# Kernel optimization log

Hardware: AMD Instinct MI355X
Metric: run time of the kernel (lower is better)

The kernel has to match this reference:

```python
import jax, jax.numpy as jnp
import numpy as np


def conv1d(x, w, b):
    # x: (N, Cin, W), w: (Cout, Cin, K) -> (N, Cout, W-K+1), VALID conv (torch Conv1d)
    y = jax.lax.conv_general_dilated(x, w, (1,), 'VALID', dimension_numbers=('NCH', 'OIH', 'NCH'))
    return y + b[None, :, None]


def cnn_block(x, w, b):
    # conv1d then MaxPool1d over the full valid length -> (N, Cout)
    return jnp.max(conv1d(x, w, b), axis=2)


def highway(x, Wp, bp, Wg, bg):
    p = jax.nn.relu(x @ Wp.T + bp)
    g = jax.nn.sigmoid(x @ Wg.T + bg)
    return g * p + (1.0 - g) * x


def lstm_masked(x, lens, Wih, Whh, bih, bhh):
    # x: (N, Wt, E); lens: (N,) valid lengths. Emulates pack_padded_sequence +
    # nn.LSTM + pad_packed_sequence: outputs are h_t for t < len, zeros after.
    N, Wt, _ = x.shape
    H = Whh.shape[1]
    bias = bih + bhh
    h0 = jnp.zeros((N, H), x.dtype)

    def step(carry, inp):
        xt, t = inp
        h, c = carry
        z = xt @ Wih.T + h @ Whh.T + bias  # (N, 4H), gate order i,f,g,o
        i, f, g, o = jnp.split(z, 4, axis=-1)
        c2 = jax.nn.sigmoid(f) * c + jax.nn.sigmoid(i) * jnp.tanh(g)
        h2 = jax.nn.sigmoid(o) * jnp.tanh(c2)
        valid = (t < lens)[:, None]
        h2 = jnp.where(valid, h2, h)
        c2 = jnp.where(valid, c2, c)
        return (h2, c2), jnp.where(valid, h2, jnp.zeros_like(h2))

    xs = jnp.moveaxis(x, 1, 0)  # (Wt, N, E)
    ts = jnp.arange(Wt)
    _, out = jax.lax.scan(step, (h0, h0), (xs, ts))
    return jnp.moveaxis(out, 0, 1)  # (N, Wt, H)


def setup_inputs() -> dict:
    key = jax.random.key(0)
    ks = jax.random.split(key, 32)
    B, T = 32, 48
    WL, WA, WE = 33, 50, 30
    EL, EA, EE, H = 300, 988, 20, 128
    CL, CA, CE = 128, 256, 64
    s = 0.02
    inp = {
        'x_lin': jax.random.normal(ks[0], (B, T, WL, EL), jnp.float32),
        'x_aco': jax.random.normal(ks[1], (B, T, WA, EA), jnp.float32),
        'x_emo': jax.random.normal(ks[2], (B, T, WE, EE), jnp.float32),
        'window_length': jax.random.randint(ks[3], (B, T), 0, WE).astype(jnp.int32) + 1,
        'length': jax.random.randint(ks[4], (B,), 1, T + 1).astype(jnp.int32),
        # CNN params
        'convL_w': s * jax.random.normal(ks[5], (CL, EL, 5), jnp.float32),
        'convL_b': jnp.zeros((CL,), jnp.float32),
        'convA_w': s * jax.random.normal(ks[6], (CA, EA, 10), jnp.float32),
        'convA_b': jnp.zeros((CA,), jnp.float32),
        'convE_w': s * jax.random.normal(ks[7], (CE, H, 3), jnp.float32),
        'convE_b': jnp.zeros((CE,), jnp.float32),
        # Highway params
        'hwL_Wp': s * jax.random.normal(ks[8], (CL, CL), jnp.float32),
        'hwL_bp': jnp.zeros((CL,), jnp.float32),
        'hwL_Wg': s * jax.random.normal(ks[9], (CL, CL), jnp.float32),
        'hwL_bg': jnp.zeros((CL,), jnp.float32),
        'hwA_Wp': s * jax.random.normal(ks[10], (CA, CA), jnp.float32),
        'hwA_bp': jnp.zeros((CA,), jnp.float32),
        'hwA_Wg': s * jax.random.normal(ks[11], (CA, CA), jnp.float32),
        'hwA_bg': jnp.zeros((CA,), jnp.float32),
        'hwE_Wp': s * jax.random.normal(ks[12], (CE, CE), jnp.float32),
        'hwE_bp': jnp.zeros((CE,), jnp.float32),
        'hwE_Wg': s * jax.random.normal(ks[13], (CE, CE), jnp.float32),
        'hwE_bg': jnp.zeros((CE,), jnp.float32),
        # LSTM params (nn.LSTM, 1 layer, batch_first)
        'lstm_Wih': s * jax.random.normal(ks[14], (4 * H, EE), jnp.float32),
        'lstm_Whh': s * jax.random.normal(ks[15], (4 * H, H), jnp.float32),
        'lstm_bih': jnp.zeros((4 * H,), jnp.float32),
        'lstm_bhh': jnp.zeros((4 * H,), jnp.float32),
    }
    return inp


def reference(x_lin, x_aco, x_emo, window_length, length,
              convL_w, convL_b, convA_w, convA_b, convE_w, convE_b,
              hwL_Wp, hwL_bp, hwL_Wg, hwL_bg,
              hwA_Wp, hwA_bp, hwA_Wg, hwA_bg,
              hwE_Wp, hwE_bp, hwE_Wg, hwE_bg,
              lstm_Wih, lstm_Whh, lstm_bih, lstm_bhh):
    B, T = x_lin.shape[:2]
    # Linguistic: per-window CNN + Highway (dropout = identity in eval)
    xl = x_lin.reshape(B * T, x_lin.shape[2], x_lin.shape[3]).transpose(0, 2, 1)  # (BT, 300, WL)
    outL = highway(cnn_block(xl, convL_w, convL_b), hwL_Wp, hwL_bp, hwL_Wg, hwL_bg)
    outL = outL.reshape(B, T, -1)
    # Acoustic
    xa = x_aco.reshape(B * T, x_aco.shape[2], x_aco.shape[3]).transpose(0, 2, 1)  # (BT, 988, WA)
    outA = highway(cnn_block(xa, convA_w, convA_b), hwA_Wp, hwA_bp, hwA_Wg, hwA_bg)
    outA = outA.reshape(B, T, -1)
    # Emotient: ragged per-window LSTM (packed semantics) -> CNN -> Highway
    xe = x_emo.reshape(B * T, x_emo.shape[2], x_emo.shape[3])  # (BT, WE, 20)
    lens = window_length.reshape(B * T)
    h = lstm_masked(xe, lens, lstm_Wih, lstm_Whh, lstm_bih, lstm_bhh)  # (BT, WE, 128)
    outE = highway(cnn_block(h.transpose(0, 2, 1), convE_w, convE_b), hwE_Wp, hwE_bp, hwE_Wg, hwE_bg)
    outE = outE.reshape(B, T, -1)
    # Concatenate modalities -> (B, T, 128+256+64) fed to the downstream head
    return jnp.concatenate([outL, outA, outE], axis=2)
```

## Files before the change

kernel.cpp:

```cpp
#include <hip/hip_runtime.h>
#include <hip/hip_bf16.h>
#include <math.h>

#define BTOT 1536
#define EL 300
#define ELP 320
#define WL_ 33
#define CL 128
#define LOUTL 29
#define KPL 1600
#define EA 988
#define EAP 992
#define WA_ 50
#define CA 256
#define LOUTA 41
#define KPA 9920
#define EE 20
#define WE_ 30
#define HH 128
#define CE 64
#define LOUTE 28
#define KPE 384
#define KDIML 1500
#define KDIMA 9880
// ... 5 lines not shown
__device__ __forceinline__ unsigned short f2bf(float f) {
    unsigned int x = __float_as_uint(f);
    unsigned int r = (x + 0x7fffu + ((x >> 16) & 1u)) >> 16;
    return (unsigned short)r;
}

__device__ __forceinline__ float sigmf(float x) {
    return __builtin_amdgcn_rcpf(1.f + __expf(-x));
}
__device__ __forceinline__ float tanh_fast(float x) {
    return 1.f - 2.f * __builtin_amdgcn_rcpf(1.f + __expf(2.f * x));
}

#define GLD16(gp, lp) __builtin_amdgcn_global_load_lds( \
    (const __attribute__((address_space(1))) void*)(gp), \
    (__attribute__((address_space(3))) void*)(lp), 16, 0, 0)

template<int N> __device__ __forceinline__ void vmwait() {
    if constexpr (N == 0) asm volatile("s_waitcnt vmcnt(0)" ::: "memory");
    else if constexpr (N == 1) asm volatile("s_waitcnt vmcnt(1)" ::: "memory");
    else if constexpr (N == 2) asm volatile("s_waitcnt vmcnt(2)" ::: "memory");
    else if constexpr (N == 3) asm volatile("s_waitcnt vmcnt(3)" ::: "memory");
    else if constexpr (N == 4) asm volatile("s_waitcnt vmcnt(4)" ::: "memory");
    else if constexpr (N == 5) asm volatile("s_waitcnt vmcnt(5)" ::: "memory");
    else if constexpr (N == 6) asm volatile("s_waitcnt vmcnt(6)" ::: "memory");
    else if constexpr (N == 8) asm volatile("s_waitcnt vmcnt(8)" ::: "memory");
    else static_assert(N == 0, "add case");
}

__device__ __forceinline__ void tr_one(const float* a, float* at, int R, int C, int idx) {
    int r = idx / C, c = idx - r * C;
    at[c * R + r] = a[idx];
}
template<int CIN, int CINP, int KW, int COUT, int KPAD>
__device__ __forceinline__ void wt_one(const float* w, unsigned short* wt, int idx) {
    int co = idx / KPAD;
    int p  = idx - co * KPAD;
    int k  = p / CINP;
    int c  = p - k * CINP;
    float v = 0.f;
    if (k < KW && c < CIN) v = w[(co * CIN + c) * KW + k];
    wt[idx] = f2bf(v);
}
template<bool BIG>
__global__ void prep_all(const float* hwL_Wp, float* WpTL, const float* hwL_Wg, float* WgTL,
                         const float* hwA_Wp, float* WpTA, const float* hwA_Wg, float* WgTA,
                         const float* hwE_Wp, float* WpTE, const float* hwE_Wg, float* WgTE,
                         const float* lstm_Wih, float* WihT, const float* lstm_Whh, float* WhhT,
                         const float* convL_w, unsigned short* wtL,
                         const float* convE_w, unsigned short* wtE,
                         const float* convA_w, unsigned short* wtA,
                         unsigned short* whh_bf, unsigned short* wihp_bf) {
    constexpr int S1 = 16384, S2 = 16384, S3 = 65536, S4 = 65536, S5 = 4096, S6 = 4096;
    constexpr int S7 = 512 * 20, S8 = 512 * 128;
    constexpr int S9 = 128 * KPL, S10 = 64 * KPE, S11 = 512 * 128, S12 = 512 * 32;
    constexpr int S13 = CA * KPA;
    constexpr int SMALL = S1 + S2 + S3 + S4 + S5 + S6 + S7 + S8;
    constexpr int TOTAL = BIG ? (SMALL + S9 + S10 + S11 + S12 + S13) : SMALL;
    int stride = gridDim.x * blockDim.x;
    for (int i = blockIdx.x * blockDim.x + threadIdx.x; i < TOTAL; i += stride) {
        int idx = i;
        if (idx < S1) { tr_one(hwL_Wp, WpTL, 128, 128, idx); continue; } idx -= S1;
        if (idx < S2) { tr_one(hwL_Wg, WgTL, 128, 128, idx); continue; } idx -= S2;
        if (idx < S3) { tr_one(hwA_Wp, WpTA, 256, 256, idx); continue; } idx -= S3;
        if (idx < S4) { tr_one(hwA_Wg, WgTA, 256, 256, idx); continue; } idx -= S4;
        if (idx < S5) { tr_one(hwE_Wp, WpTE, 64, 64, idx); continue; } idx -= S5;
        if (idx < S6) { tr_one(hwE_Wg, WgTE, 64, 64, idx); continue; } idx -= S6;
        if (idx < S7) { tr_one(lstm_Wih, WihT, 512, 20, idx); continue; } idx -= S7;
        if (idx < S8) { tr_one(lstm_Whh, WhhT, 512, 128, idx); continue; } idx -= S8;
        if constexpr (BIG) {
            if (idx < S9) { wt_one<EL, ELP, 5, CL, KPL>(convL_w, wtL, idx); continue; } idx -= S9;
            if (idx < S10) { wt_one<HH, HH, 3, CE, KPE>(convE_w, wtE, idx); continue; } idx -= S10;
            if (idx < S11) { whh_bf[idx] = f2bf(lstm_Whh[idx]); continue; } idx -= S11;
            if (idx < S12) { int col = idx >> 5, e = idx & 31;
                             wihp_bf[idx] = (e < 20) ? f2bf(lstm_Wih[col * 20 + e]) : (unsigned short)0;
                             continue; } idx -= S12;
            wt_one<EA, EAP, 10, CA, KPA>(convA_w, wtA, idx);
        }
    }
}

template<int CIN, int CINP>
__device__ __forceinline__ void cvt_chunk(const float* in, unsigned short* out, int idx) {
    constexpr int CH = CINP / 8;
    int row = idx / CH, c0 = (idx - row * CH) * 8;
    const float* src = in + (size_t)row * CIN + c0;
    union { short8 s; unsigned short u[8]; } o;
    if (c0 + 8 <= CIN) {
        float4 v0 = *(const float4*)src;
        float4 v1 = *(const float4*)(src + 4);
        o.u[0]=f2bf(v0.x); o.u[1]=f2bf(v0.y); o.u[2]=f2bf(v0.z); o.u[3]=f2bf(v0.w);
        o.u[4]=f2bf(v1.x); o.u[5]=f2bf(v1.y); o.u[6]=f2bf(v1.z); o.u[7]=f2bf(v1.w);
    } else {
        #pragma unroll
        for (int j = 0; j < 8; ++j) o.u[j] = (c0 + j < CIN) ? f2bf(src[j]) : (unsigned short)0;
    }
    *(short8*)(out + (size_t)row * CINP + c0) = o.s;
}

#define LSTM_BLOCKS 96
#define CVTA_BLOCKS 1440

__global__ __launch_bounds__(512, 1)
void lstm_cvt(const float* __restrict__ x_emo,
              const unsigned short* __restrict__ wihp_bf, const unsigned short* __restrict__ whh_bf,
              const float* __restrict__ bih, const float* __restrict__ bhh,
              const int* __restrict__ lens, unsigned short* __restrict__ hbuf,
              const float* __restrict__ xa, unsigned short* __restrict__ outa)
{
    __shared__ __align__(16) unsigned short xq[WE_ * 16 * 32];
    __shared__ __align__(16) char h_s[2 * 16 * HH * 2];

    if (blockIdx.x >= LSTM_BLOCKS) {
        constexpr int NAC = (BTOT * WA_) * (EAP / 8);
        int stride = CVTA_BLOCKS * 512;
        for (int i = (blockIdx.x - LSTM_BLOCKS) * 512 + threadIdx.x; i < NAC; i += stride)
            cvt_chunk<EA, EAP>(xa, outa, i);
        return;
    }

    const int tid  = threadIdx.x;
    const int w    = tid >> 6;
    const int lane = tid & 63;
    const int lr   = lane & 15;
    const int lq   = lane >> 4;
    const int s0   = blockIdx.x * 16;
    const int c    = w * 16 + lr;

    short8 bfr[4][4];
    short8 bw[4];
    float bj[4];
    #pragma unroll
    for (int g = 0; g < 4; ++g) {
        int col = g * 128 + c;
        #pragma unroll
        for (int kt = 0; kt < 4; ++kt)
            bfr[g][kt] = *(const short8*)(whh_bf + (size_t)col * 128 + kt * 32 + lq * 8);
        bw[g] = *(const short8*)(wihp_bf + (size_t)col * 32 + lq * 8);
        bj[g] = bih[col] + bhh[col];
    }
    int len4[4];
    #pragma unroll
    for (int j = 0; j < 4; ++j) len4[j] = lens[s0 + lq * 4 + j];

    for (int i = tid; i < WE_ * 16 * 32; i += 512) {
        int t = i >> 9, r = (i >> 5) & 15, e = i & 31;
        xq[i] = (e < 20) ? f2bf(x_emo[(((size_t)(s0 + r) * WE_) + t) * 20 + e]) : (unsigned short)0;
    }
    for (int i = tid; i < 2048; i += 512) ((unsigned int*)h_s)[i] = 0u;

    float c_prev[4] = {0.f, 0.f, 0.f, 0.f};
    unsigned short hb_prev[4] = {0, 0, 0, 0};
    __syncthreads();

    for (int t = 0; t < WE_; ++t) {
        const char* hsr = h_s + (t & 1) * 4096;
        char* hsw = h_s + ((t & 1) ^ 1) * 4096;
        short8 ax = *(const short8*)((const char*)xq + (size_t)(t * 16 + lr) * 64 + lq * 16);
        short8 af[4];
        #pragma unroll
        for (int kt = 0; kt < 4; ++kt)
// ... 10 lines not shown
        #pragma unroll
        for (int j = 0; j < 4; ++j) {
            int s = lq * 4 + j;
            float zi = acc[0][j] + bj[0];
            float zf = acc[1][j] + bj[1];
            float zg = acc[2][j] + bj[2];
            float zo = acc[3][j] + bj[3];
            float si = sigmf(zi), sf = sigmf(zf), so = sigmf(zo);
            float tg = tanh_fast(zg);
            float c2 = sf * c_prev[j] + si * tg;
            float h2 = so * tanh_fast(c2);
            bool valid = (t < len4[j]);
            c_prev[j] = valid ? c2 : c_prev[j];
            unsigned short h2b = f2bf(h2);
            unsigned short hn = valid ? h2b : hb_prev[j];
            hb_prev[j] = hn;
            *(unsigned short*)(hsw + (((s * HH + c) * 2) ^ ((s & 7) << 4))) = hn;
            hbuf[(((size_t)(s0 + s) * WE_) + t) * HH + c] = valid ? h2b : (unsigned short)0;
        }
        __syncthreads();
    }
}

#define CONVA_BLOCKS 768
#define CVTL_BLOCKS 512
__global__ __launch_bounds__(256, 2)
void conv_a_v11(const unsigned short* __restrict__ xb, const unsigned short* __restrict__ wt,
                const float* __restrict__ bias, float* __restrict__ pooled,
                const float* __restrict__ xl, unsigned short* __restrict__ outl)
{
    constexpr int LOUT = LOUTA, WIN = WA_, CINP = EAP, BN = 128, COUT = CA;
    constexpr int CCH  = CINP / 32;
    constexpr int KB   = CINP * 2;
    constexpr int KTOTB = CINP * 10 * 2;
    constexpr int ABUF = 4 * 64 * 64;
    constexpr int BBUF = BN * 64;
    constexpr int CPQ  = 96;

    __shared__ __align__(16) char smem[2 * ABUF + 5 * BBUF];

    if (blockIdx.x >= CONVA_BLOCKS) {
        constexpr int NLC = (BTOT * WL_) * (ELP / 8);
        int stride = CVTL_BLOCKS * 256;
        for (int i = (blockIdx.x - CONVA_BLOCKS) * 256 + threadIdx.x; i < NLC; i += stride)
            cvt_chunk<EL, ELP>(xl, outl, i);
        return;
    }

    const int tid  = threadIdx.x;
    const int lane = tid & 63;
    const int wid  = tid >> 6;
    const int lr   = lane & 15;
    const int lq   = lane >> 4;
    const int lq16 = lq * 16;

    int xcd = blockIdx.x & 7;
    int n = xcd & 1;
    int m = (xcd >> 1) * CPQ + (blockIdx.x >> 3);

    f32x4 acc[3][8];
    #pragma unroll
    for (int i = 0; i < 3; ++i)
        #pragma unroll
        for (int j = 0; j < 8; ++j) acc[i][j] = (f32x4){0.f, 0.f, 0.f, 0.f};

    const int aw_r = tid >> 2;
    const int aw   = (aw_r < WIN) ? aw_r : (WIN - 1);
    const int slot = tid & 3;
    const char* asrc[4];
    #pragma unroll
    for (int i = 0; i < 4; ++i)
        asrc[i] = (const char*)xb + ((size_t)((m * 4 + i) * WIN + aw)) * KB
                + ((slot * 16) ^ (((aw_r >> 1) & 3) << 4));
    const char* bsrc[2];
    #pragma unroll
    for (int i = 0; i < 2; ++i) {
        int col = (tid + i * 256) >> 2;
        bsrc[i] = (const char*)wt + (size_t)(n * BN + col) * KTOTB
                + ((slot * 16) ^ (((col >> 1) & 3) << 4));
    }

// ... 87 lines not shown
    }
#undef VSTEP

    const int bt = m * 4 + wid;
    #pragma unroll
    for (int nf = 0; nf < 8; ++nf) {
        float mx = -INFINITY;
        #pragma unroll
        for (int o = 0; o < 3; ++o) {
            int rb = o * 16 + lq * 4;
            #pragma unroll
            for (int j = 0; j < 4; ++j)
                if (rb + j < LOUT) mx = fmaxf(mx, acc[o][nf][j]);
        }
        mx = fmaxf(mx, __shfl_xor(mx, 16, 64));
        mx = fmaxf(mx, __shfl_xor(mx, 32, 64));
        if (lane < 16) {
            int col = n * BN + nf * 16 + lane;
            pooled[(size_t)bt * COUT + col] = mx + bias[col];
        }
    }
}

template<int LOUT, int WIN, int CINP, int KW, int BN, int NS, int MFR, int COUT>
__global__ __launch_bounds__(256, 2)
void conv_pool_v10(const unsigned short* __restrict__ xb, const unsigned short* __restrict__ wt,
                   const float* __restrict__ bias, float* __restrict__ pooled)
{
    constexpr int CCH   = CINP / 32;
    constexpr int KB    = CINP * 2;
    constexpr int KTOTB = CINP * KW * 2;
    constexpr int NFR   = BN / 16;
    constexpr int B_IT  = BN / 64;
    constexpr int ABUF  = 4 * 64 * 64;
    constexpr int BBUF  = BN * 64;
    constexpr int CPQ   = (BTOT / 4) / 4;

    __shared__ __align__(16) char smem[2 * ABUF + 4 * BBUF];

    const int tid  = threadIdx.x;
    const int lane = tid & 63;
    const int wid  = tid >> 6;
    const int lr   = lane & 15;
    const int lq   = lane >> 4;
    const int lq16 = lq * 16;

    int m, n;
    if constexpr (NS == 2) {
        int xcd = blockIdx.x & 7;
        n = xcd & 1;
        m = (xcd >> 1) * CPQ + (blockIdx.x >> 3);
    } else {
        m = blockIdx.x; n = 0;
    }

    f32x4 acc[MFR][NFR];
    #pragma unroll
    for (int i = 0; i < MFR; ++i)
        #pragma unroll
        for (int j = 0; j < NFR; ++j) acc[i][j] = (f32x4){0.f, 0.f, 0.f, 0.f};

    const int aw_r = tid >> 2;
    const int aw   = (aw_r < WIN) ? aw_r : (WIN - 1);
    const int slot = tid & 3;
    const char* asrc[4];
    #pragma unroll
    for (int i = 0; i < 4; ++i)
        asrc[i] = (const char*)xb + ((size_t)((m * 4 + i) * WIN + aw)) * KB
                + ((slot * 16) ^ (((aw_r >> 1) & 3) << 4));
    const char* bsrc[B_IT];
    #pragma unroll
    for (int i = 0; i < B_IT; ++i) {
        int col = (tid + i * 256) >> 2;
        bsrc[i] = (const char*)wt + (size_t)(n * BN + col) * KTOTB
                + ((slot * 16) ^ (((col >> 1) & 3) << 4));
    }

    char* const abuf0 = smem;
    char* const abuf1 = smem + ABUF;
    char* const bbase = smem + 2 * ABUF;

    int cbo[NFR];
    #pragma unroll
    for (int nf = 0; nf < NFR; ++nf) {
        int cb = nf * 16 + lr;
        cbo[nf] = cb * 64 + (lq16 ^ (((cb >> 1) & 3) << 4));
    }

    #pragma unroll
    for (int i = 0; i < 4; ++i)
        GLD16(asrc[i], abuf0 + i * 4096 + tid * 16);
    #pragma unroll
    for (int s = 0; s < 3; ++s)
        #pragma unroll
        for (int i = 0; i < B_IT; ++i)
            GLD16(bsrc[i] + s * KB, bbase + s * BBUF + i * 4096 + tid * 16);
    vmwait<0>();
    __builtin_amdgcn_s_barrier();

    int bcur = 0;

#define STEP(KK, WN, TAIL) do {                                                    \
    const char* bb = bbase + bcur * BBUF;                                          \
    short8 afr[MFR];                                                               \
    _Pragma("unroll")                                                              \
    for (int o = 0; o < MFR; ++o) {                                                \
        int row = o * 16 + lr + (KK);                                              \
        afr[o] = *(const short8*)(awave + row * 64 + (lq16 ^ (((row >> 1) & 3) << 4))); \
    }                                                                              \
    short8 bf[NFR];                                                                \
    _Pragma("unroll")                                                              \
    for (int nf = 0; nf < NFR; ++nf) bf[nf] = *(const short8*)(bb + cbo[nf]);      \
    if (!(TAIL) || (KK) < KW - 3) {                                                \
        constexpr int k3_ = ((KK) + 3 < KW) ? (KK) + 3 : (KK) + 3 - KW;            \
        int boff = k3_ * KB + (((KK) + 3 < KW) ? ci : ci + 1) * 64;                \
        char* bstg = bbase + ((bcur + 3) & 3) * BBUF;                              \
        _Pragma("unroll")                                                          \
        for (int i = 0; i < B_IT; ++i)                                             \
            GLD16(bsrc[i] + boff, bstg + i * 4096 + tid * 16);                     \
    }                                                                              \
    if (!(TAIL)) {                                                                 \
        if (KW >= 8) {                                                             \
            if ((KK) < 4)                                                          \
                GLD16(asrc[(KK) & 3] + (size_t)(ci + 1) * 64, abn + ((KK) & 3) * 4096 + tid * 16); \
        } else if ((KK) == 0) {                                                    \
            _Pragma("unroll")                                                      \
            for (int i = 0; i < 4; ++i)                                            \
                GLD16(asrc[i] + (size_t)(ci + 1) * 64, abn + i * 4096 + tid * 16); \
        }                                                                          \
    }                                                                              \
    __builtin_amdgcn_s_setprio(1);                                                 \
    _Pragma("unroll")                                                              \
    for (int nf = 0; nf < NFR; ++nf)                                               \
        _Pragma("unroll")                                                          \
        for (int o = 0; o < MFR; ++o)                                              \
            acc[o][nf] = __builtin_amdgcn_mfma_f32_16x16x32_bf16(afr[o], bf[nf], acc[o][nf], 0, 0, 0); \
    __builtin_amdgcn_s_setprio(0);                                                 \
    vmwait<WN>();                                                                  \
    asm volatile("" ::: "memory");                                                 \
    __builtin_amdgcn_s_barrier();                                                  \
    bcur = (bcur + 1) & 3;                                                         \
} while (0)

    for (int ci = 0; ci < CCH - 1; ++ci) {
        const char* ab = (ci & 1) ? abuf1 : abuf0;
        char* abn = (ci & 1) ? abuf0 : abuf1;
        const char* awave = ab + wid * 4096;
        if constexpr (KW == 5) {
            STEP(0, 8, false); STEP(1, 8, false); STEP(2, 4, false); STEP(3, 4, false); STEP(4, 4, false);
        } else {
            STEP(0, 6, false); STEP(1, 6, false); STEP(2, 2, false);
        }
    }
    {
        const int ci = CCH - 1;
        const char* ab = (ci & 1) ? abuf1 : abuf0;
        char* abn = (ci & 1) ? abuf0 : abuf1; (void)abn;
        const char* awave = ab + wid * 4096;
        if constexpr (KW == 5) {
            STEP(0, 4, true); STEP(1, 4, true); STEP(2, 2, true); STEP(3, 0, true); STEP(4, 0, true);
        } else {
            STEP(0, 1, true); STEP(1, 0, true); STEP(2, 0, true);
        }
    }
#undef STEP

    const int bt = m * 4 + wid;
    #pragma unroll
    for (int nf = 0; nf < NFR; ++nf) {
        float mx = -INFINITY;
        #pragma unroll
        for (int o = 0; o < MFR; ++o) {
            int rb = o * 16 + lq * 4;
            #pragma unroll
            for (int j = 0; j < 4; ++j)
                if (rb + j < LOUT) mx = fmaxf(mx, acc[o][nf][j]);
        }
        mx = fmaxf(mx, __shfl_xor(mx, 16, 64));
        mx = fmaxf(mx, __shfl_xor(mx, 32, 64));
        if (lane < 16) {
            int col = n * BN + nf * 16 + lane;
            pooled[(size_t)bt * COUT + col] = mx + bias[col];
        }
    }
}

#define HWA_BLOCKS 192
#define HWL_BLOCKS 96
#define HWE_BLOCKS 48
__global__ __launch_bounds__(256)
void highway_v2(const float* __restrict__ pL, const float* __restrict__ pA, const float* __restrict__ pE,
                const float* __restrict__ WpTL, const float* __restrict__ bpL,
                const float* __restrict__ WgTL, const float* __restrict__ bgL,
                const float* __restrict__ WpTA, const float* __restrict__ bpA,
                const float* __restrict__ WgTA, const float* __restrict__ bgA,
                const float* __restrict__ WpTE, const float* __restrict__ bpE,
                const float* __restrict__ WgTE, const float* __restrict__ bgE,
                float* __restrict__ out) {
    __shared__ float xs[2048];
    int bx = blockIdx.x;
    int tid = threadIdx.x;
    if (bx < HWA_BLOCKS) {
        int bt0 = bx * 8;
        #pragma unroll
        for (int s = 0; s < 8; ++s) xs[s * 256 + tid] = pA[(size_t)(bt0 + s) * 256 + tid];
        __syncthreads();
// ... 38 lines not shown
        }
    } else {
        int bt0 = (bx - HWA_BLOCKS - HWL_BLOCKS) * 32;
        for (int i = tid; i < 32 * 64; i += 256) xs[i] = pE[(size_t)bt0 * 64 + i];
        __syncthreads();
        int j = tid & 63, grp = tid >> 6;
        float p[8], g[8];
        #pragma unroll
        for (int s = 0; s < 8; ++s) { p[s] = bpE[j]; g[s] = bgE[j]; }
        for (int c = 0; c < 64; ++c) {
            float wp = WpTE[c * 64 + j], wg = WgTE[c * 64 + j];
            #pragma unroll
            for (int s = 0; s < 8; ++s) {
                float xv = xs[(grp * 8 + s) * 64 + c];
                p[s] += xv * wp; g[s] += xv * wg;
            }
        }
        #pragma unroll
        for (int s = 0; s < 8; ++s) {
            float pp = fmaxf(p[s], 0.f);
            float gg = sigmf(g[s]);
            out[(size_t)(bt0 + grp * 8 + s) * 448 + 384 + j] = gg * pp + (1.f - gg) * xs[(grp * 8 + s) * 64 + j];
        }
    }
}

__global__ __launch_bounds__(512)
void lstm_kernel_f32(const float* __restrict__ x, const int* __restrict__ lens,
                     const float* __restrict__ WihT, const float* __restrict__ WhhT,
                     const float* __restrict__ bih, const float* __restrict__ bhh,
                     float* __restrict__ hout) {
    int bt = blockIdx.x;
    int j  = threadIdx.x;
    __shared__ float xs[WE_][EE];
    __shared__ __align__(16) float hs[HH];
    __shared__ float zs[512];
    for (int idx = j; idx < WE_ * EE; idx += 512)
        ((float*)xs)[idx] = x[(size_t)bt * WE_ * EE + idx];
    if (j < HH) hs[j] = 0.f;
    float wih[EE];
    #pragma unroll
    for (int e = 0; e < EE; ++e) wih[e] = WihT[e * 512 + j];
    float whh[HH];
    #pragma unroll
    for (int h = 0; h < HH; ++h) whh[h] = WhhT[h * 512 + j];
    float bjv = bih[j] + bhh[j];
// ... 84 lines not shown
    const float* hwA_Wg = (const float*)d_in[17];
    const float* hwA_bg = (const float*)d_in[18];
    const float* hwE_Wp = (const float*)d_in[19];
    const float* hwE_bp = (const float*)d_in[20];
    const float* hwE_Wg = (const float*)d_in[21];
    const float* hwE_bg = (const float*)d_in[22];
    const float* lstm_Wih = (const float*)d_in[23];
    const float* lstm_Whh = (const float*)d_in[24];
    const float* lstm_bih = (const float*)d_in[25];
    const float* lstm_bhh = (const float*)d_in[26];
    float* out = (float*)d_out;

    char* p0 = (char*)d_ws;
    char* p = p0;
    auto alloc = [&](size_t bytes) { char* r = p; p += (bytes + 255) & ~(size_t)255; return r; };
    float* WpTL = (float*)alloc((size_t)CL * CL * 4);
    float* WgTL = (float*)alloc((size_t)CL * CL * 4);
    float* WpTA = (float*)alloc((size_t)CA * CA * 4);
    float* WgTA = (float*)alloc((size_t)CA * CA * 4);
    float* WpTE = (float*)alloc((size_t)CE * CE * 4);
    float* WgTE = (float*)alloc((size_t)CE * CE * 4);
    float* WihT = (float*)alloc((size_t)EE * 512 * 4);
    float* WhhT = (float*)alloc((size_t)HH * 512 * 4);
    unsigned short* whh_bf  = (unsigned short*)alloc((size_t)512 * 128 * 2);
    unsigned short* wihp_bf = (unsigned short*)alloc((size_t)512 * 32 * 2);
    void*  hbuf = (void*)alloc((size_t)BTOT * WE_ * HH * 4);
    float* pL   = (float*)alloc((size_t)BTOT * CL * 4);
    float* pA   = (float*)alloc((size_t)BTOT * CA * 4);
    float* pE   = (float*)alloc((size_t)BTOT * CE * 4);
    unsigned short* wtA = (unsigned short*)alloc((size_t)CA * KPA * 2);
    unsigned short* wtL = (unsigned short*)alloc((size_t)CL * KPL * 2);
    unsigned short* wtE = (unsigned short*)alloc((size_t)CE * KPE * 2);
    unsigned short* xlin_p = (unsigned short*)alloc((size_t)BTOT * WL_ * ELP * 2 + 64);
    unsigned short* xaco_p = (unsigned short*)alloc((size_t)BTOT * WA_ * EAP * 2 + 64);
    size_t need = (size_t)(p - p0);
    bool big = ws_size >= need;

    if (big) {
        prep_all<true><<<2048, 256, 0, stream>>>(hwL_Wp, WpTL, hwL_Wg, WgTL, hwA_Wp, WpTA, hwA_Wg, WgTA,
                                                 hwE_Wp, WpTE, hwE_Wg, WgTE, lstm_Wih, WihT, lstm_Whh, WhhT,
                                                 convL_w, wtL, convE_w, wtE, convA_w, wtA, whh_bf, wihp_bf);
        lstm_cvt<<<LSTM_BLOCKS + CVTA_BLOCKS, 512, 0, stream>>>(
            x_emo, wihp_bf, whh_bf, lstm_bih, lstm_bhh, wlen, (unsigned short*)hbuf,
            x_aco, xaco_p);
        conv_a_v11<<<CONVA_BLOCKS + CVTL_BLOCKS, 256, 0, stream>>>(
            xaco_p, wtA, convA_b, pA, x_lin, xlin_p);
        conv_pool_v10<LOUTL, WL_, ELP, 5, 128, 1, 2, CL>
            <<<384, 256, 0, stream>>>(xlin_p, wtL, convL_b, pL);
        conv_pool_v10<LOUTE, WE_, HH, 3, 64, 1, 2, CE>
            <<<384, 256, 0, stream>>>((const unsigned short*)hbuf, wtE, convE_b, pE);
        highway_v2<<<HWA_BLOCKS + HWL_BLOCKS + HWE_BLOCKS, 256, 0, stream>>>(
            pL, pA, pE, WpTL, hwL_bp, WgTL, hwL_bg, WpTA, hwA_bp, WgTA, hwA_bg,
            WpTE, hwE_bp, WgTE, hwE_bg, out);
    } else {
        prep_all<false><<<2048, 256, 0, stream>>>(hwL_Wp, WpTL, hwL_Wg, WgTL, hwA_Wp, WpTA, hwA_Wg, WgTA,
                                                  hwE_Wp, WpTE, hwE_Wg, WgTE, lstm_Wih, WihT, lstm_Whh, WhhT,
                                                  convL_w, wtL, convE_w, wtE, convA_w, wtA, whh_bf, wihp_bf);
        lstm_kernel_f32<<<BTOT, 512, 0, stream>>>(x_emo, wlen, WihT, WhhT, lstm_bih, lstm_bhh, (float*)hbuf);
        conv_pool_simple<EA, WA_, CA, KDIMA, LOUTA>
            <<<dim3(BTOT, CA / 64), 256, 0, stream>>>(x_aco, convA_w, convA_b, pA);
        conv_pool_simple<EL, WL_, CL, KDIML, LOUTL>
            <<<dim3(BTOT, CL / 64), 256, 0, stream>>>(x_lin, convL_w, convL_b, pL);
        conv_pool_simple<HH, WE_, CE, KDIME, LOUTE>
            <<<dim3(BTOT, CE / 64), 256, 0, stream>>>((const float*)hbuf, convE_w, convE_b, pE);
        highway_v2<<<HWA_BLOCKS + HWL_BLOCKS + HWE_BLOCKS, 256, 0, stream>>>(
            pL, pA, pE, WpTL, hwL_bp, WgTL, hwL_bg, WpTA, hwA_bp, WgTA, hwA_bg,
            WpTE, hwE_bp, WgTE, hwE_bg, out);
    }
}
```

Measured before the change: 518.6 us.

## Merge prep, LSTM, input conversion and all convs into fewer launches

The weight-prep kernel is folded into the LSTM/convert kernel as extra grid-stride work. The LSTM blocks now convert their own Whh/Wih weights to bf16 directly from fp32, so they no longer wait on a separate prep launch. The linguistic input conversion moves into that same kernel, and the three conv+pool kernels (acoustic, linguistic, emotient) are combined into one conv_all launch that dispatches on block index. The aim is to cut the launch count from six to three and let the independent stages share one wave of the GPU, at the cost of a heavier auxiliary kernel and mixed block types inside one grid.

Measured after the change: 538.0 us. +3.7%, slower.

```diff
diff --git a/kernel.cpp b/kernel.cpp
--- a/kernel.cpp
+++ b/kernel.cpp
@@ -51,7 +51,6 @@
     else if constexpr (N == 2) asm volatile("s_waitcnt vmcnt(2)" ::: "memory");
     else if constexpr (N == 3) asm volatile("s_waitcnt vmcnt(3)" ::: "memory");
     else if constexpr (N == 4) asm volatile("s_waitcnt vmcnt(4)" ::: "memory");
-    else if constexpr (N == 5) asm volatile("s_waitcnt vmcnt(5)" ::: "memory");
     else if constexpr (N == 6) asm volatile("s_waitcnt vmcnt(6)" ::: "memory");
     else if constexpr (N == 8) asm volatile("s_waitcnt vmcnt(8)" ::: "memory");
     else static_assert(N == 0, "add case");
@@ -71,44 +70,6 @@
     if (k < KW && c < CIN) v = w[(co * CIN + c) * KW + k];
     wt[idx] = f2bf(v);
 }
-template<bool BIG>
-__global__ void prep_all(const float* hwL_Wp, float* WpTL, const float* hwL_Wg, float* WgTL,
-                         const float* hwA_Wp, float* WpTA, const float* hwA_Wg, float* WgTA,
-                         const float* hwE_Wp, float* WpTE, const float* hwE_Wg, float* WgTE,
-                         const float* lstm_Wih, float* WihT, const float* lstm_Whh, float* WhhT,
-                         const float* convL_w, unsigned short* wtL,
-                         const float* convE_w, unsigned short* wtE,
-                         const float* convA_w, unsigned short* wtA,
-                         unsigned short* whh_bf, unsigned short* wihp_bf) {
-    constexpr int S1 = 16384, S2 = 16384, S3 = 65536, S4 = 65536, S5 = 4096, S6 = 4096;
-    constexpr int S7 = 512 * 20, S8 = 512 * 128;
-    constexpr int S9 = 128 * KPL, S10 = 64 * KPE, S11 = 512 * 128, S12 = 512 * 32;
-    constexpr int S13 = CA * KPA;
-    constexpr int SMALL = S1 + S2 + S3 + S4 + S5 + S6 + S7 + S8;
-    constexpr int TOTAL = BIG ? (SMALL + S9 + S10 + S11 + S12 + S13) : SMALL;
-    int stride = gridDim.x * blockDim.x;
-    for (int i = blockIdx.x * blockDim.x + threadIdx.x; i < TOTAL; i += stride) {
-        int idx = i;
-        if (idx < S1) { tr_one(hwL_Wp, WpTL, 128, 128, idx); continue; } idx -= S1;
-        if (idx < S2) { tr_one(hwL_Wg, WgTL, 128, 128, idx); continue; } idx -= S2;
-        if (idx < S3) { tr_one(hwA_Wp, WpTA, 256, 256, idx); continue; } idx -= S3;
-        if (idx < S4) { tr_one(hwA_Wg, WgTA, 256, 256, idx); continue; } idx -= S4;
-        if (idx < S5) { tr_one(hwE_Wp, WpTE, 64, 64, idx); continue; } idx -= S5;
-        if (idx < S6) { tr_one(hwE_Wg, WgTE, 64, 64, idx); continue; } idx -= S6;
-        if (idx < S7) { tr_one(lstm_Wih, WihT, 512, 20, idx); continue; } idx -= S7;
-        if (idx < S8) { tr_one(lstm_Whh, WhhT, 512, 128, idx); continue; } idx -= S8;
-        if constexpr (BIG) {
-            if (idx < S9) { wt_one<EL, ELP, 5, CL, KPL>(convL_w, wtL, idx); continue; } idx -= S9;
-            if (idx < S10) { wt_one<HH, HH, 3, CE, KPE>(convE_w, wtE, idx); continue; } idx -= S10;
-            if (idx < S11) { whh_bf[idx] = f2bf(lstm_Whh[idx]); continue; } idx -= S11;
-            if (idx < S12) { int col = idx >> 5, e = idx & 31;
-                             wihp_bf[idx] = (e < 20) ? f2bf(lstm_Wih[col * 20 + e]) : (unsigned short)0;
-                             continue; } idx -= S12;
-            wt_one<EA, EAP, 10, CA, KPA>(convA_w, wtA, idx);
-        }
-    }
-}
-
 template<int CIN, int CINP>
 __device__ __forceinline__ void cvt_chunk(const float* in, unsigned short* out, int idx) {
     constexpr int CH = CINP / 8;
@@ -128,23 +89,46 @@
 }
 
 #define LSTM_BLOCKS 96
-#define CVTA_BLOCKS 1440
+#define AUX_BLOCKS 1952
 
 __global__ __launch_bounds__(512, 1)
-void lstm_cvt(const float* __restrict__ x_emo,
-              const unsigned short* __restrict__ wihp_bf, const unsigned short* __restrict__ whh_bf,
-              const float* __restrict__ bih, const float* __restrict__ bhh,
-              const int* __restrict__ lens, unsigned short* __restrict__ hbuf,
-              const float* __restrict__ xa, unsigned short* __restrict__ outa)
+void lstm_cvt_prep(const float* __restrict__ x_emo,
+                   const float* __restrict__ lstm_Wih, const float* __restrict__ lstm_Whh,
+                   const float* __restrict__ bih, const float* __restrict__ bhh,
+                   const int* __restrict__ lens, unsigned short* __restrict__ hbuf,
+                   const float* __restrict__ xa, const float* __restrict__ xl,
+                   unsigned short* __restrict__ outa, unsigned short* __restrict__ outl,
+                   const float* hwL_Wp, float* WpTL, const float* hwL_Wg, float* WgTL,
+                   const float* hwA_Wp, float* WpTA, const float* hwA_Wg, float* WgTA,
+                   const float* hwE_Wp, float* WpTE, const float* hwE_Wg, float* WgTE,
+                   const float* convL_w, unsigned short* wtL,
+                   const float* convE_w, unsigned short* wtE,
+                   const float* convA_w, unsigned short* wtA)
 {
     __shared__ __align__(16) unsigned short xq[WE_ * 16 * 32];
     __shared__ __align__(16) char h_s[2 * 16 * HH * 2];
 
     if (blockIdx.x >= LSTM_BLOCKS) {
         constexpr int NAC = (BTOT * WA_) * (EAP / 8);
-        int stride = CVTA_BLOCKS * 512;
-        for (int i = (blockIdx.x - LSTM_BLOCKS) * 512 + threadIdx.x; i < NAC; i += stride)
-            cvt_chunk<EA, EAP>(xa, outa, i);
+        constexpr int NLC = (BTOT * WL_) * (ELP / 8);
+        constexpr int S1 = 16384, S2 = 16384, S3 = 65536, S4 = 65536, S5 = 4096, S6 = 4096;
+        constexpr int S9 = 128 * KPL, S10 = 64 * KPE, S13 = CA * KPA;
+        constexpr int TOTAL = NAC + NLC + S1 + S2 + S3 + S4 + S5 + S6 + S9 + S10 + S13;
+        int stride = AUX_BLOCKS * 512;
+        for (int i = (blockIdx.x - LSTM_BLOCKS) * 512 + threadIdx.x; i < TOTAL; i += stride) {
+            int idx = i;
+            if (idx < NAC) { cvt_chunk<EA, EAP>(xa, outa, idx); continue; } idx -= NAC;
+            if (idx < NLC) { cvt_chunk<EL, ELP>(xl, outl, idx); continue; } idx -= NLC;
+            if (idx < S1) { tr_one(hwL_Wp, WpTL, 128, 128, idx); continue; } idx -= S1;
+            if (idx < S2) { tr_one(hwL_Wg, WgTL, 128, 128, idx); continue; } idx -= S2;
+            if (idx < S3) { tr_one(hwA_Wp, WpTA, 256, 256, idx); continue; } idx -= S3;
+            if (idx < S4) { tr_one(hwA_Wg, WgTA, 256, 256, idx); continue; } idx -= S4;
+            if (idx < S5) { tr_one(hwE_Wp, WpTE, 64, 64, idx); continue; } idx -= S5;
+            if (idx < S6) { tr_one(hwE_Wg, WgTE, 64, 64, idx); continue; } idx -= S6;
+            if (idx < S9) { wt_one<EL, ELP, 5, CL, KPL>(convL_w, wtL, idx); continue; } idx -= S9;
+            if (idx < S10) { wt_one<HH, HH, 3, CE, KPE>(convE_w, wtE, idx); continue; } idx -= S10;
+            wt_one<EA, EAP, 10, CA, KPA>(convA_w, wtA, idx);
+        }
         return;
     }
 
@@ -163,9 +147,22 @@
     for (int g = 0; g < 4; ++g) {
         int col = g * 128 + c;
         #pragma unroll
-        for (int kt = 0; kt < 4; ++kt)
-            bfr[g][kt] = *(const short8*)(whh_bf + (size_t)col * 128 + kt * 32 + lq * 8);
-        bw[g] = *(const short8*)(wihp_bf + (size_t)col * 32 + lq * 8);
+        for (int kt = 0; kt < 4; ++kt) {
+            const float* s = lstm_Whh + (size_t)col * 128 + kt * 32 + lq * 8;
+            float4 v0 = *(const float4*)s;
+            float4 v1 = *(const float4*)(s + 4);
+            union { short8 sv; unsigned short u[8]; } o;
+            o.u[0]=f2bf(v0.x); o.u[1]=f2bf(v0.y); o.u[2]=f2bf(v0.z); o.u[3]=f2bf(v0.w);
+            o.u[4]=f2bf(v1.x); o.u[5]=f2bf(v1.y); o.u[6]=f2bf(v1.z); o.u[7]=f2bf(v1.w);
+            bfr[g][kt] = o.sv;
+        }
+        union { short8 sv; unsigned short u[8]; } ow;
+        #pragma unroll
+        for (int j = 0; j < 8; ++j) {
+            int e = lq * 8 + j;
+            ow.u[j] = (e < 20) ? f2bf(lstm_Wih[(size_t)col * 20 + e]) : (unsigned short)0;
+        }
+        bw[g] = ow.sv;
         bj[g] = bih[col] + bhh[col];
     }
     int len4[4];
@@ -222,12 +219,159 @@
     }
 }
 
-#define CONVA_BLOCKS 768
-#define CVTL_BLOCKS 512
-__global__ __launch_bounds__(256, 2)
-void conv_a_v11(const unsigned short* __restrict__ xb, const unsigned short* __restrict__ wt,
-                const float* __restrict__ bias, float* __restrict__ pooled,
-                const float* __restrict__ xl, unsigned short* __restrict__ outl)
+template<int LOUT, int WIN, int CINP, int KW, int BN, int MFR, int COUT>
+__device__ __forceinline__
+void conv_body_v10(char* smem, int m, int n,
+                   const unsigned short* __restrict__ xb, const unsigned short* __restrict__ wt,
+                   const float* __restrict__ bias, float* __restrict__ pooled)
+{
+    constexpr int CCH   = CINP / 32;
+    constexpr int KB    = CINP * 2;
+    constexpr int KTOTB = CINP * KW * 2;
+    constexpr int NFR   = BN / 16;
+    constexpr int B_IT  = BN / 64;
+    constexpr int ABUF  = 4 * 64 * 64;
+    constexpr int BBUF  = BN * 64;
+
+    const int tid  = threadIdx.x;
+    const int lane = tid & 63;
+    const int wid  = tid >> 6;
+    const int lr   = lane & 15;
+    const int lq   = lane >> 4;
+    const int lq16 = lq * 16;
+
+    f32x4 acc[MFR][NFR];
+    #pragma unroll
+    for (int i = 0; i < MFR; ++i)
+        #pragma unroll
+        for (int j = 0; j < NFR; ++j) acc[i][j] = (f32x4){0.f, 0.f, 0.f, 0.f};
+
+    const int aw_r = tid >> 2;
+    const int aw   = (aw_r < WIN) ? aw_r : (WIN - 1);
+    const int slot = tid & 3;
+    const char* asrc[4];
+    #pragma unroll
+    for (int i = 0; i < 4; ++i)
+        asrc[i] = (const char*)xb + ((size_t)((m * 4 + i) * WIN + aw)) * KB
+                + ((slot * 16) ^ (((aw_r >> 1) & 3) << 4));
+    const char* bsrc[B_IT];
+    #pragma unroll
+    for (int i = 0; i < B_IT; ++i) {
+        int col = (tid + i * 256) >> 2;
+        bsrc[i] = (const char*)wt + (size_t)(n * BN + col) * KTOTB
+                + ((slot * 16) ^ (((col >> 1) & 3) << 4));
+    }
+
+    char* const abuf0 = smem;
+    char* const abuf1 = smem + ABUF;
+    char* const bbase = smem + 2 * ABUF;
+
+    int cbo[NFR];
+    #pragma unroll
+    for (int nf = 0; nf < NFR; ++nf) {
+        int cb = nf * 16 + lr;
+        cbo[nf] = cb * 64 + (lq16 ^ (((cb >> 1) & 3) << 4));
+    }
+
+    #pragma unroll
+    for (int i = 0; i < 4; ++i)
+        GLD16(asrc[i], abuf0 + i * 4096 + tid * 16);
+    #pragma unroll
+    for (int s = 0; s < 3; ++s)
+        #pragma unroll
+        for (int i = 0; i < B_IT; ++i)
+            GLD16(bsrc[i] + s * KB, bbase + s * BBUF + i * 4096 + tid * 16);
+    vmwait<0>();
+    __builtin_amdgcn_s_barrier();
+
+    int bcur = 0;
+
+#define STEP(KK, WN, TAIL) do {                                                    \
+    const char* bb = bbase + bcur * BBUF;                                          \
+    short8 afr[MFR];                                                               \
+    _Pragma("unroll")                                                              \
+    for (int o = 0; o < MFR; ++o) {                                                \
+        int row = o * 16 + lr + (KK);                                              \
+        afr[o] = *(const short8*)(awave + row * 64 + (lq16 ^ (((row >> 1) & 3) << 4))); \
+    }                                                                              \
+    short8 bf[NFR];                                                                \
+    _Pragma("unroll")                                                              \
+    for (int nf = 0; nf < NFR; ++nf) bf[nf] = *(const short8*)(bb + cbo[nf]);      \
+    if (!(TAIL) || (KK) < KW - 3) {                                                \
+        constexpr int k3_ = ((KK) + 3 < KW) ? (KK) + 3 : (KK) + 3 - KW;            \
+        int boff = k3_ * KB + (((KK) + 3 < KW) ? ci : ci + 1) * 64;                \
+        char* bstg = bbase + ((bcur + 3) & 3) * BBUF;                              \
+        _Pragma("unroll")                                                          \
+        for (int i = 0; i < B_IT; ++i)                                             \
+            GLD16(bsrc[i] + boff, bstg + i * 4096 + tid * 16);                     \
+    }                                                                              \
+    if (!(TAIL)) {                                                                 \
+        if ((KK) == 0) {                                                           \
+            _Pragma("unroll")                                                      \
+            for (int i = 0; i < 4; ++i)                                            \
+                GLD16(asrc[i] + (size_t)(ci + 1) * 64, abn + i * 4096 + tid * 16); \
+        }                                                                          \
+    }                                                                              \
+    __builtin_amdgcn_s_setprio(1);                                                 \
+    _Pragma("unroll")                                                              \
+    for (int nf = 0; nf < NFR; ++nf)                                               \
+        _Pragma("unroll")                                                          \
+        for (int o = 0; o < MFR; ++o)                                              \
+            acc[o][nf] = __builtin_amdgcn_mfma_f32_16x16x32_bf16(afr[o], bf[nf], acc[o][nf], 0, 0, 0); \
+    __builtin_amdgcn_s_setprio(0);                                                 \
+    vmwait<WN>();                                                                  \
+    asm volatile("" ::: "memory");                                                 \
+    __builtin_amdgcn_s_barrier();                                                  \
+    bcur = (bcur + 1) & 3;                                                         \
+} while (0)
+
+    for (int ci = 0; ci < CCH - 1; ++ci) {
+        const char* ab = (ci & 1) ? abuf1 : abuf0;
+        char* abn = (ci & 1) ? abuf0 : abuf1;
+        const char* awave = ab + wid * 4096;
+        if constexpr (KW == 5) {
+            STEP(0, 8, false); STEP(1, 8, false); STEP(2, 4, false); STEP(3, 4, false); STEP(4, 4, false);
+        } else {
+            STEP(0, 6, false); STEP(1, 6, false); STEP(2, 2, false);
+        }
+    }
+    {
+        const int ci = CCH - 1;
+        const char* ab = (ci & 1) ? abuf1 : abuf0;
+        char* abn = (ci & 1) ? abuf0 : abuf1; (void)abn;
+        const char* awave = ab + wid * 4096;
+        if constexpr (KW == 5) {
+            STEP(0, 4, true); STEP(1, 4, true); STEP(2, 2, true); STEP(3, 0, true); STEP(4, 0, true);
+        } else {
+            STEP(0, 1, true); STEP(1, 0, true); STEP(2, 0, true);
+        }
+    }
+#undef STEP
+
+    const int bt = m * 4 + wid;
+    #pragma unroll
+    for (int nf = 0; nf < NFR; ++nf) {
+        float mx = -INFINITY;
+        #pragma unroll
+        for (int o = 0; o < MFR; ++o) {
+            int rb = o * 16 + lq * 4;
+            #pragma unroll
+            for (int j = 0; j < 4; ++j)
+                if (rb + j < LOUT) mx = fmaxf(mx, acc[o][nf][j]);
+        }
+        mx = fmaxf(mx, __shfl_xor(mx, 16, 64));
+        mx = fmaxf(mx, __shfl_xor(mx, 32, 64));
+        if (lane < 16) {
+            int col = n * BN + nf * 16 + lane;
+            pooled[(size_t)bt * COUT + col] = mx + bias[col];
+        }
+    }
+}
+
+__device__ __forceinline__
+void conv_body_a(char* smem, int m, int n,
+                 const unsigned short* __restrict__ xb, const unsigned short* __restrict__ wt,
+                 const float* __restrict__ bias, float* __restrict__ pooled)
 {
     constexpr int LOUT = LOUTA, WIN = WA_, CINP = EAP, BN = 128, COUT = CA;
     constexpr int CCH  = CINP / 32;
@@ -235,17 +379,6 @@
     constexpr int KTOTB = CINP * 10 * 2;
     constexpr int ABUF = 4 * 64 * 64;
     constexpr int BBUF = BN * 64;
-    constexpr int CPQ  = 96;
-
-    __shared__ __align__(16) char smem[2 * ABUF + 5 * BBUF];
-
-    if (blockIdx.x >= CONVA_BLOCKS) {
-        constexpr int NLC = (BTOT * WL_) * (ELP / 8);
-        int stride = CVTL_BLOCKS * 256;
-        for (int i = (blockIdx.x - CONVA_BLOCKS) * 256 + threadIdx.x; i < NLC; i += stride)
-            cvt_chunk<EL, ELP>(xl, outl, i);
-        return;
-    }
 
     const int tid  = threadIdx.x;
     const int lane = tid & 63;
@@ -253,10 +386,6 @@
     const int lr   = lane & 15;
     const int lq   = lane >> 4;
     const int lq16 = lq * 16;
-
-    int xcd = blockIdx.x & 7;
-    int n = xcd & 1;
-    int m = (xcd >> 1) * CPQ + (blockIdx.x >> 3);
 
     f32x4 acc[3][8];
     #pragma unroll
@@ -390,166 +519,29 @@
     }
 }
 
-template<int LOUT, int WIN, int CINP, int KW, int BN, int NS, int MFR, int COUT>
+#define CONVA_BLOCKS 768
+#define CONVL_BLOCKS 384
 __global__ __launch_bounds__(256, 2)
-void conv_pool_v10(const unsigned short* __restrict__ xb, const unsigned short* __restrict__ wt,
-                   const float* __restrict__ bias, float* __restrict__ pooled)
+void conv_all(const unsigned short* __restrict__ xaco_p, const unsigned short* __restrict__ wtA,
+              const float* __restrict__ convA_b, float* __restrict__ pA,
+              const unsigned short* __restrict__ xlin_p, const unsigned short* __restrict__ wtL,
+              const float* __restrict__ convL_b, float* __restrict__ pL,
+              const unsigned short* __restrict__ hbuf, const unsigned short* __restrict__ wtE,
+              const float* __restrict__ convE_b, float* __restrict__ pE)
 {
-    constexpr int CCH   = CINP / 32;
-    constexpr int KB    = CINP * 2;
-    constexpr int KTOTB = CINP * KW * 2;
-    constexpr int NFR   = BN / 16;
-    constexpr int B_IT  = BN / 64;
-    constexpr int ABUF  = 4 * 64 * 64;
-    constexpr int BBUF  = BN * 64;
-    constexpr int CPQ   = (BTOT / 4) / 4;
-
-    __shared__ __align__(16) char smem[2 * ABUF + 4 * BBUF];
-
-    const int tid  = threadIdx.x;
-    const int lane = tid & 63;
-    const int wid  = tid >> 6;
-    const int lr   = lane & 15;
-    const int lq   = lane >> 4;
-    const int lq16 = lq * 16;
-
-    int m, n;
-    if constexpr (NS == 2) {
-        int xcd = blockIdx.x & 7;
-        n = xcd & 1;
-        m = (xcd >> 1) * CPQ + (blockIdx.x >> 3);
+    __shared__ __align__(16) char smem[73728];
+    int bx = blockIdx.x;
+    if (bx < CONVA_BLOCKS) {
+        int xcd = bx & 7;
+        int n = xcd & 1;
+        int m = (xcd >> 1) * 96 + (bx >> 3);
+        conv_body_a(smem, m, n, xaco_p, wtA, convA_b, pA);
+    } else if (bx < CONVA_BLOCKS + CONVL_BLOCKS) {
+        conv_body_v10<LOUTL, WL_, ELP, 5, 128, 2, CL>(smem, bx - CONVA_BLOCKS, 0,
+                                                      xlin_p, wtL, convL_b, pL);
     } else {
-        m = blockIdx.x; n = 0;
-    }
-
-    f32x4 acc[MFR][NFR];
-    #pragma unroll
-    for (int i = 0; i < MFR; ++i)
-        #pragma unroll
-        for (int j = 0; j < NFR; ++j) acc[i][j] = (f32x4){0.f, 0.f, 0.f, 0.f};
-
-    const int aw_r = tid >> 2;
-    const int aw   = (aw_r < WIN) ? aw_r : (WIN - 1);
-    const int slot = tid & 3;
-    const char* asrc[4];
-    #pragma unroll
-    for (int i = 0; i < 4; ++i)
-        asrc[i] = (const char*)xb + ((size_t)((m * 4 + i) * WIN + aw)) * KB
-                + ((slot * 16) ^ (((aw_r >> 1) & 3) << 4));
-    const char* bsrc[B_IT];
-    #pragma unroll
-    for (int i = 0; i < B_IT; ++i) {
-        int col = (tid + i * 256) >> 2;
-        bsrc[i] = (const char*)wt + (size_t)(n * BN + col) * KTOTB
-                + ((slot * 16) ^ (((col >> 1) & 3) << 4));
-    }
-
-    char* const abuf0 = smem;
-    char* const abuf1 = smem + ABUF;
-    char* const bbase = smem + 2 * ABUF;
-
-    int cbo[NFR];
-    #pragma unroll
-    for (int nf = 0; nf < NFR; ++nf) {
-        int cb = nf * 16 + lr;
-        cbo[nf] = cb * 64 + (lq16 ^ (((cb >> 1) & 3) << 4));
-    }
-
-    #pragma unroll
-    for (int i = 0; i < 4; ++i)
-        GLD16(asrc[i], abuf0 + i * 4096 + tid * 16);
-    #pragma unroll
-    for (int s = 0; s < 3; ++s)
-        #pragma unroll
-        for (int i = 0; i < B_IT; ++i)
-            GLD16(bsrc[i] + s * KB, bbase + s * BBUF + i * 4096 + tid * 16);
-    vmwait<0>();
-    __builtin_amdgcn_s_barrier();
-
-    int bcur = 0;
-
-#define STEP(KK, WN, TAIL) do {                                                    \
-    const char* bb = bbase + bcur * BBUF;                                          \
-    short8 afr[MFR];                                                               \
-    _Pragma("unroll")                                                              \
-    for (int o = 0; o < MFR; ++o) {                                                \
-        int row = o * 16 + lr + (KK);                                              \
-        afr[o] = *(const short8*)(awave + row * 64 + (lq16 ^ (((row >> 1) & 3) << 4))); \
-    }                                                                              \
-    short8 bf[NFR];                                                                \
-    _Pragma("unroll")                                                              \
-    for (int nf = 0; nf < NFR; ++nf) bf[nf] = *(const short8*)(bb + cbo[nf]);      \
-    if (!(TAIL) || (KK) < KW - 3) {                                                \
-        constexpr int k3_ = ((KK) + 3 < KW) ? (KK) + 3 : (KK) + 3 - KW;            \
-        int boff = k3_ * KB + (((KK) + 3 < KW) ? ci : ci + 1) * 64;                \
-        char* bstg = bbase + ((bcur + 3) & 3) * BBUF;                              \
-        _Pragma("unroll")                                                          \
-        for (int i = 0; i < B_IT; ++i)                                             \
-            GLD16(bsrc[i] + boff, bstg + i * 4096 + tid * 16);                     \
-    }                                                                              \
-    if (!(TAIL)) {                                                                 \
-        if (KW >= 8) {                                                             \
-            if ((KK) < 4)                                                          \
-                GLD16(asrc[(KK) & 3] + (size_t)(ci + 1) * 64, abn + ((KK) & 3) * 4096 + tid * 16); \
-        } else if ((KK) == 0) {                                                    \
-            _Pragma("unroll")                                                      \
-            for (int i = 0; i < 4; ++i)                                            \
-                GLD16(asrc[i] + (size_t)(ci + 1) * 64, abn + i * 4096 + tid * 16); \
-        }                                                                          \
-    }                                                                              \
-    __builtin_amdgcn_s_setprio(1);                                                 \
-    _Pragma("unroll")                                                              \
-    for (int nf = 0; nf < NFR; ++nf)                                               \
-        _Pragma("unroll")                                                          \
-        for (int o = 0; o < MFR; ++o)                                              \
-            acc[o][nf] = __builtin_amdgcn_mfma_f32_16x16x32_bf16(afr[o], bf[nf], acc[o][nf], 0, 0, 0); \
-    __builtin_amdgcn_s_setprio(0);                                                 \
-    vmwait<WN>();                                                                  \
-    asm volatile("" ::: "memory");                                                 \
-    __builtin_amdgcn_s_barrier();                                                  \
-    bcur = (bcur + 1) & 3;                                                         \
-} while (0)
-
-    for (int ci = 0; ci < CCH - 1; ++ci) {
-        const char* ab = (ci & 1) ? abuf1 : abuf0;
-        char* abn = (ci & 1) ? abuf0 : abuf1;
-        const char* awave = ab + wid * 4096;
-        if constexpr (KW == 5) {
-            STEP(0, 8, false); STEP(1, 8, false); STEP(2, 4, false); STEP(3, 4, false); STEP(4, 4, false);
-        } else {
-            STEP(0, 6, false); STEP(1, 6, false); STEP(2, 2, false);
-        }
-    }
-    {
-        const int ci = CCH - 1;
-        const char* ab = (ci & 1) ? abuf1 : abuf0;
-        char* abn = (ci & 1) ? abuf0 : abuf1; (void)abn;
-        const char* awave = ab + wid * 4096;
-        if constexpr (KW == 5) {
-            STEP(0, 4, true); STEP(1, 4, true); STEP(2, 2, true); STEP(3, 0, true); STEP(4, 0, true);
-        } else {
-            STEP(0, 1, true); STEP(1, 0, true); STEP(2, 0, true);
-        }
-    }
-#undef STEP
-
-    const int bt = m * 4 + wid;
-    #pragma unroll
-    for (int nf = 0; nf < NFR; ++nf) {
-        float mx = -INFINITY;
-        #pragma unroll
-        for (int o = 0; o < MFR; ++o) {
-            int rb = o * 16 + lq * 4;
-            #pragma unroll
-            for (int j = 0; j < 4; ++j)
-                if (rb + j < LOUT) mx = fmaxf(mx, acc[o][nf][j]);
-        }
-        mx = fmaxf(mx, __shfl_xor(mx, 16, 64));
-        mx = fmaxf(mx, __shfl_xor(mx, 32, 64));
-        if (lane < 16) {
-            int col = n * BN + nf * 16 + lane;
-            pooled[(size_t)bt * COUT + col] = mx + bias[col];
-        }
+        conv_body_v10<LOUTE, WE_, HH, 3, 64, 2, CE>(smem, bx - CONVA_BLOCKS - CONVL_BLOCKS, 0,
+                                                    hbuf, wtE, convE_b, pE);
     }
 }
 
@@ -634,6 +626,27 @@
             float gg = sigmf(g[s]);
             out[(size_t)(bt0 + grp * 8 + s) * 448 + 384 + j] = gg * pp + (1.f - gg) * xs[(grp * 8 + s) * 64 + j];
         }
+    }
+}
+
+__global__ void prep_fallback(const float* hwL_Wp, float* WpTL, const float* hwL_Wg, float* WgTL,
+                              const float* hwA_Wp, float* WpTA, const float* hwA_Wg, float* WgTA,
+                              const float* hwE_Wp, float* WpTE, const float* hwE_Wg, float* WgTE,
+                              const float* lstm_Wih, float* WihT, const float* lstm_Whh, float* WhhT) {
+    constexpr int S1 = 16384, S2 = 16384, S3 = 65536, S4 = 65536, S5 = 4096, S6 = 4096;
+    constexpr int S7 = 512 * 20, S8 = 512 * 128;
+    constexpr int TOTAL = S1 + S2 + S3 + S4 + S5 + S6 + S7 + S8;
+    int stride = gridDim.x * blockDim.x;
+    for (int i = blockIdx.x * blockDim.x + threadIdx.x; i < TOTAL; i += stride) {
+        int idx = i;
+        if (idx < S1) { tr_one(hwL_Wp, WpTL, 128, 128, idx); continue; } idx -= S1;
+        if (idx < S2) { tr_one(hwL_Wg, WgTL, 128, 128, idx); continue; } idx -= S2;
+        if (idx < S3) { tr_one(hwA_Wp, WpTA, 256, 256, idx); continue; } idx -= S3;
+        if (idx < S4) { tr_one(hwA_Wg, WgTA, 256, 256, idx); continue; } idx -= S4;
+        if (idx < S5) { tr_one(hwE_Wp, WpTE, 64, 64, idx); continue; } idx -= S5;
+        if (idx < S6) { tr_one(hwE_Wg, WgTE, 64, 64, idx); continue; } idx -= S6;
+        if (idx < S7) { tr_one(lstm_Wih, WihT, 512, 20, idx); continue; } idx -= S7;
+        tr_one(lstm_Whh, WhhT, 512, 128, idx);
     }
 }
 
@@ -764,8 +777,6 @@
     float* WgTE = (float*)alloc((size_t)CE * CE * 4);
     float* WihT = (float*)alloc((size_t)EE * 512 * 4);
     float* WhhT = (float*)alloc((size_t)HH * 512 * 4);
-    unsigned short* whh_bf  = (unsigned short*)alloc((size_t)512 * 128 * 2);
-    unsigned short* wihp_bf = (unsigned short*)alloc((size_t)512 * 32 * 2);
     void*  hbuf = (void*)alloc((size_t)BTOT * WE_ * HH * 4);
     float* pL   = (float*)alloc((size_t)BTOT * CL * 4);
     float* pA   = (float*)alloc((size_t)BTOT * CA * 4);
@@ -779,25 +790,20 @@
     bool big = ws_size >= need;
 
     if (big) {
-        prep_all<true><<<2048, 256, 0, stream>>>(hwL_Wp, WpTL, hwL_Wg, WgTL, hwA_Wp, WpTA, hwA_Wg, WgTA,
-                                                 hwE_Wp, WpTE, hwE_Wg, WgTE, lstm_Wih, WihT, lstm_Whh, WhhT,
-                                                 convL_w, wtL, convE_w, wtE, convA_w, wtA, whh_bf, wihp_bf);
-        lstm_cvt<<<LSTM_BLOCKS + CVTA_BLOCKS, 512, 0, stream>>>(
-            x_emo, wihp_bf, whh_bf, lstm_bih, lstm_bhh, wlen, (unsigned short*)hbuf,
-            x_aco, xaco_p);
-        conv_a_v11<<<CONVA_BLOCKS + CVTL_BLOCKS, 256, 0, stream>>>(
-            xaco_p, wtA, convA_b, pA, x_lin, xlin_p);
-        conv_pool_v10<LOUTL, WL_, ELP, 5, 128, 1, 2, CL>
-            <<<384, 256, 0, stream>>>(xlin_p, wtL, convL_b, pL);
-        conv_pool_v10<LOUTE, WE_, HH, 3, 64, 1, 2, CE>
-            <<<384, 256, 0, stream>>>((const unsigned short*)hbuf, wtE, convE_b, pE);
+        lstm_cvt_prep<<<LSTM_BLOCKS + AUX_BLOCKS, 512, 0, stream>>>(
+            x_emo, lstm_Wih, lstm_Whh, lstm_bih, lstm_bhh, wlen, (unsigned short*)hbuf,
+            x_aco, x_lin, xaco_p, xlin_p,
+            hwL_Wp, WpTL, hwL_Wg, WgTL, hwA_Wp, WpTA, hwA_Wg, WgTA, hwE_Wp, WpTE, hwE_Wg, WgTE,
+            convL_w, wtL, convE_w, wtE, convA_w, wtA);
+        conv_all<<<1536, 256, 0, stream>>>(xaco_p, wtA, convA_b, pA,
+                                           xlin_p, wtL, convL_b, pL,
+                                           (const unsigned short*)hbuf, wtE, convE_b, pE);
         highway_v2<<<HWA_BLOCKS + HWL_BLOCKS + HWE_BLOCKS, 256, 0, stream>>>(
             pL, pA, pE, WpTL, hwL_bp, WgTL, hwL_bg, WpTA, hwA_bp, WgTA, hwA_bg,
             WpTE, hwE_bp, WgTE, hwE_bg, out);
     } else {
-        prep_all<false><<<2048, 256, 0, stream>>>(hwL_Wp, WpTL, hwL_Wg, WgTL, hwA_Wp, WpTA, hwA_Wg, WgTA,
-                                                  hwE_Wp, WpTE, hwE_Wg, WgTE, lstm_Wih, WihT, lstm_Whh, WhhT,
-                                                  convL_w, wtL, convE_w, wtE, convA_w, wtA, whh_bf, wihp_bf);
+        prep_fallback<<<512, 256, 0, stream>>>(hwL_Wp, WpTL, hwL_Wg, WgTL, hwA_Wp, WpTA, hwA_Wg, WgTA,
+                                               hwE_Wp, WpTE, hwE_Wg, WgTE, lstm_Wih, WihT, lstm_Whh, WhhT);
         lstm_kernel_f32<<<BTOT, 512, 0, stream>>>(x_emo, wlen, WihT, WhhT, lstm_bih, lstm_bhh, (float*)hbuf);
         conv_pool_simple<EA, WA_, CA, KDIMA, LOUTA>
             <<<dim3(BTOT, CA / 64), 256, 0, stream>>>(x_aco, convA_w, convA_b, pA);
```
